# Kernel optimization log

Measured on AMD Instinct MI355X. Metric: run time of the kernel, lower is better.

## Reference

```python
import jax, jax.numpy as jnp
import numpy as np

B, S, E, H = 4, 2048, 1024, 8
D = E // H  # head_dim = 128


def setup_inputs() -> dict:
    key = jax.random.key(0)
    ks = jax.random.split(key, 7)
    scale = 1.0 / np.sqrt(D)
    return {
        "sequences": jax.random.normal(ks[0], (B, S, E), dtype=jnp.float32),
        # per-head Linear weights, torch layout [out, in] stacked over heads
        "Wq": jax.random.normal(ks[1], (H, D, D), dtype=jnp.float32) * scale,
        "Wk": jax.random.normal(ks[2], (H, D, D), dtype=jnp.float32) * scale,
        "Wv": jax.random.normal(ks[3], (H, D, D), dtype=jnp.float32) * scale,
        "bq": jax.random.normal(ks[4], (H, D), dtype=jnp.float32) * scale,
        "bk": jax.random.normal(ks[5], (H, D), dtype=jnp.float32) * scale,
        "bv": jax.random.normal(ks[6], (H, D), dtype=jnp.float32) * scale,
    }


def reference(sequences, Wq, Wk, Wv, bq, bk, bv):
    # split feature dim into heads: [B,S,H,D]
    xh = sequences.reshape(B, S, H, D)
    # torch Linear: y = x @ W.T + b  ->  contract input dim d with W[h, o, d]
    q = jnp.einsum("bshd,hod->bsho", xh, Wq) + bq
    k = jnp.einsum("bshd,hod->bsho", xh, Wk) + bk
    v = jnp.einsum("bshd,hod->bsho", xh, Wv) + bv
    # NOTE: original scales by 1/sqrt(num_heads), not 1/sqrt(head_dim)
    scores = jnp.einsum("bshd,bthd->bhst", q, k) / jnp.sqrt(jnp.float32(H))
    attn = jax.nn.softmax(scores, axis=-1)  # [B,H,S,S]
    out = jnp.einsum("bhst,bthd->bshd", attn, v)
    # hstack over heads == reshape back to [B,S,E]
    return out.reshape(B, S, E)
```

## Files before the change

### kernel.cpp

```cpp
#include <hip/hip_runtime.h>
#include <hip/hip_bf16.h>

#define B_ 4
#define S_ 2048
#define E_ 1024
#define H_ 8
#define D_ 128

using f16x8 = __attribute__((ext_vector_type(8))) _Float16;
using f32x4 = __attribute__((ext_vector_type(4))) float;

__device__ __forceinline__ ushort f2h_bits(float f) {
    union { _Float16 h; ushort u; } cv; cv.h = (_Float16)f; return cv.u;
}
__device__ __forceinline__ f16x8 pack8(const float* __restrict__ p) {
    float4 f0 = *(const float4*)p;
    float4 f1 = *(const float4*)(p + 4);
    f16x8 r;
    r[0] = (_Float16)f0.x; r[1] = (_Float16)f0.y;
    r[2] = (_Float16)f0.z; r[3] = (_Float16)f0.w;
    r[4] = (_Float16)f1.x; r[5] = (_Float16)f1.y;
    r[6] = (_Float16)f1.z; r[7] = (_Float16)f1.w;
    return r;
}

__device__ __forceinline__ void gll16(const ushort* g, ushort* l) {
    __builtin_amdgcn_global_load_lds(
        (const __attribute__((address_space(1))) unsigned int*)g,
        (__attribute__((address_space(3))) unsigned int*)l, 16, 0, 0);
}

__global__ __launch_bounds__(256) void kv_proj(
    const float* __restrict__ seq,
    const float* __restrict__ Wk, const float* __restrict__ Wv,
    const float* __restrict__ bk, const float* __restrict__ bv,
    ushort* __restrict__ ko, ushort* __restrict__ vo)
{
    __shared__ ushort T[128 * 68];
    const int m0 = blockIdx.x * 64, h = blockIdx.y;
    const int tid = threadIdx.x, lane = tid & 63, w = tid >> 6;
    const int l16 = lane & 15, quad = lane >> 4;

    f16x8 a[4];
    #pragma unroll
    for (int ks = 0; ks < 4; ++ks)
        a[ks] = pack8(&seq[(size_t)(m0 + w * 16 + l16) * E_
                           + h * D_ + ks * 32 + quad * 8]);

    {
        const float* W = Wk + (size_t)h * D_ * D_;
        f32x4 acc[8];
        #pragma unroll
        for (int nt = 0; nt < 8; ++nt) { f32x4 z = {0.f,0.f,0.f,0.f}; acc[nt] = z; }
        #pragma unroll
        for (int ks = 0; ks < 4; ++ks)
            #pragma unroll
            for (int nt = 0; nt < 8; ++nt) {
                f16x8 bfr = pack8(&W[(size_t)(nt * 16 + l16) * D_ + ks * 32 + quad * 8]);
                acc[nt] = __builtin_amdgcn_mfma_f32_16x16x32_f16(
                    a[ks], bfr, acc[nt], 0, 0, 0);
            }
        #pragma unroll
        for (int nt = 0; nt < 8; ++nt) {
            int o = nt * 16 + l16;
            float bias = bk[h * D_ + o];
            #pragma unroll
            for (int r = 0; r < 4; ++r) {
                int row = w * 16 + quad * 4 + r;
                T[row * 136 + (o ^ (quad << 3))] = f2h_bits(acc[nt][r] + bias);
            }
        }
    }
    __syncthreads();
    #pragma unroll
    for (int i = 0; i < 4; ++i) {
        int idx = tid + i * 256;
        int row = idx >> 4, c8 = (idx & 15) * 8;
        int lk = c8 ^ ((row & 7) << 3);
        uint4 dk = *(uint4*)&T[row * 136 + (lk ^ (((row >> 2) & 3) << 3))];
        int m = m0 + row, bi = m >> 11, s = m & (S_ - 1);
        *(uint4*)&ko[(((size_t)bi * H_ + h) * S_ + s) * D_ + c8] = dk;
    }
    __syncthreads();
    {
        const float* W = Wv + (size_t)h * D_ * D_;
        f32x4 acc[8];
        #pragma unroll
        for (int nt = 0; nt < 8; ++nt) { f32x4 z = {0.f,0.f,0.f,0.f}; acc[nt] = z; }
        #pragma unroll
        for (int ks = 0; ks < 4; ++ks)
            #pragma unroll
            for (int nt = 0; nt < 8; ++nt) {
                f16x8 bfr = pack8(&W[(size_t)(nt * 16 + l16) * D_ + ks * 32 + quad * 8]);
                acc[nt] = __builtin_amdgcn_mfma_f32_16x16x32_f16(
                    a[ks], bfr, acc[nt], 0, 0, 0);
            }
        #pragma unroll
        for (int nt = 0; nt < 8; ++nt) {
            int o = nt * 16 + l16;
            float bias = bv[h * D_ + o];
            #pragma unroll
            for (int r = 0; r < 4; ++r) {
                int row = w * 16 + quad * 4 + r;
                T[o * 68 + row] = f2h_bits(acc[nt][r] + bias);
            }
        }
    }
    __syncthreads();
    #pragma unroll
    for (int i = 0; i < 4; ++i) {
        int idx = tid + i * 256;
        int d = idx >> 3, c = idx & 7;
        uint4 dv = *(uint4*)&T[d * 68 + ((c ^ (d & 7)) << 3)];
        int bi = m0 >> 11, s0 = (m0 & (S_ - 1)) + c * 8;
        *(uint4*)&vo[(((size_t)bi * H_ + h) * D_ + d) * S_ + s0] = dv;
    }
}

__global__ __launch_bounds__(512) void attn(
    const float* __restrict__ seq, const float* __restrict__ Wq,
    const float* __restrict__ bq,
    const ushort* __restrict__ kg, const ushort* __restrict__ vtg,
    float* __restrict__ out)
{
    constexpr int NT = S_ / 64;
    __shared__ alignas(16) ushort Kbuf[2][64 * 128];
    __shared__ alignas(16) ushort Vbuf[2][128 * 64];
    __shared__ alignas(16) ushort Pbuf[128 * 64];

    const int m0 = blockIdx.x * 128;
    const int h = blockIdx.y, bi = blockIdx.z;
    const int bh = bi * H_ + h;
    const int tid = threadIdx.x, lane = tid & 63, w = tid >> 6;
    const int l16 = lane & 15, quad = lane >> 4;
    const int swz = l16 & 7;
    const ushort* kbase = kg + (size_t)bh * S_ * D_;
    const ushort* vbase = vtg + (size_t)bh * D_ * S_;
    const float qscale = 0.35355339059327373f * 1.4426950408889634f;

    #pragma unroll
    for (int c = 0; c < 2; ++c) {
        int i = w * 2 + c;
        gll16(vbase + (size_t)(i * 8 + (lane >> 3)) * S_ + (lane & 7) * 8,
              &Vbuf[0][0] + i * 512);
    }

    ushort* const Qs = &Kbuf[0][0];
    {
        f16x8 xa[4];
        #pragma unroll
        for (int ks = 0; ks < 4; ++ks)
            xa[ks] = pack8(&seq[((size_t)bi * S_ + m0 + w * 16 + l16) * E_
                                + h * D_ + ks * 32 + quad * 8]);
        f32x4 qacc[8];
        #pragma unroll
        for (int nt = 0; nt < 8; ++nt) { f32x4 z = {0.f,0.f,0.f,0.f}; qacc[nt] = z; }
        const float* W = Wq + (size_t)h * D_ * D_;
        #pragma unroll
        for (int ks = 0; ks < 4; ++ks)
            #pragma unroll
            for (int nt = 0; nt < 8; ++nt) {
                f16x8 bfr = pack8(&W[(size_t)(nt * 16 + l16) * D_ + ks * 32 + quad * 8]);
                qacc[nt] = __builtin_amdgcn_mfma_f32_16x16x32_f16(
                    xa[ks], bfr, qacc[nt], 0, 0, 0);
            }
        #pragma unroll
        for (int nt = 0; nt < 8; ++nt) {
            int o = nt * 16 + l16;
            float bias = bq[h * D_ + o];
            #pragma unroll
            for (int r = 0; r < 4; ++r) {
                int row = w * 16 + quad * 4 + r;
                Qs[row * 128 + (o ^ (quad << 3))] =
                    f2h_bits((qacc[nt][r] + bias) * qscale);
            }
        }
    }
    __syncthreads();

    f16x8 qf[4];
    #pragma unroll
    for (int ks = 0; ks < 4; ++ks)
        qf[ks] = *(const f16x8*)&Qs[(w * 16 + l16) * 128
                                    + ks * 32 + ((quad ^ (l16 >> 2)) << 3)];
    __syncthreads();

    #pragma unroll
    for (int c = 0; c < 2; ++c) {
        int i = w * 2 + c;
        gll16(kbase + i * 512 + lane * 8, &Kbuf[0][0] + i * 512);
    }

    f32x4 o_acc[8];
    #pragma unroll
    for (int nt = 0; nt < 8; ++nt) { f32x4 z = {0.f,0.f,0.f,0.f}; o_acc[nt] = z; }
    float m_prev = -1e30f, l_lane = 0.f;

    __syncthreads();

    ushort* const prow = &Pbuf[(w * 16 + l16) * 64];

    for (int j = 0; j < NT; ++j) {
        const int cur = j & 1;
        const ushort* KL = &Kbuf[cur][0];
        const ushort* VL = &Vbuf[cur][0];

        if (j + 1 < NT) {
            const ushort* kt = kbase + (size_t)(j + 1) * 64 * 128;
            const ushort* vt = vbase + (j + 1) * 64;
            ushort* kd = &Kbuf[cur ^ 1][0];
            ushort* vd = &Vbuf[cur ^ 1][0];
            #pragma unroll
            for (int c = 0; c < 2; ++c) {
                int i = w * 2 + c;
                gll16(kt + i * 512 + lane * 8, kd + i * 512);
                gll16(vt + (size_t)(i * 8 + (lane >> 3)) * S_ + (lane & 7) * 8,
                      vd + i * 512);
            }
        }

        f32x4 sacc[4];
        #pragma unroll
        for (int nt = 0; nt < 4; ++nt) { f32x4 z = {0.f,0.f,0.f,0.f}; sacc[nt] = z; }
        __builtin_amdgcn_s_setprio(1);
        #pragma unroll
        for (int ks = 0; ks < 4; ++ks)
            #pragma unroll
            for (int nt = 0; nt < 4; ++nt) {
                f16x8 kf = *(const f16x8*)&KL[(nt * 16 + l16) * 128
                                              + (((ks * 4 + quad) ^ swz) << 3)];
                sacc[nt] = __builtin_amdgcn_mfma_f32_16x16x32_f16(
                    kf, qf[ks], sacc[nt], 0, 0, 0);
            }
        __builtin_amdgcn_s_setprio(0);

        uint2 pkw[4];
        {
            float mx = fmaxf(fmaxf(sacc[0][0], sacc[0][1]), fmaxf(sacc[0][2], sacc[0][3]));
            #pragma unroll
            for (int nt = 1; nt < 4; ++nt)
                mx = fmaxf(mx, fmaxf(fmaxf(sacc[nt][0], sacc[nt][1]),
                                     fmaxf(sacc[nt][2], sacc[nt][3])));
            mx = fmaxf(mx, __shfl_xor(mx, 16));
            mx = fmaxf(mx, __shfl_xor(mx, 32));
            if (__any(mx > m_prev + 8.0f)) {
                float mnew  = fmaxf(m_prev, mx);
                float alpha = exp2f(m_prev - mnew);
                #pragma unroll
                for (int nt = 0; nt < 8; ++nt)
                    #pragma unroll
                    for (int r = 0; r < 4; ++r) o_acc[nt][r] *= alpha;
                l_lane *= alpha;
                m_prev = mnew;
            }
            #pragma unroll
            for (int nt = 0; nt < 4; ++nt) {
                float e0 = exp2f(sacc[nt][0] - m_prev);
                float e1 = exp2f(sacc[nt][1] - m_prev);
                float e2 = exp2f(sacc[nt][2] - m_prev);
                float e3 = exp2f(sacc[nt][3] - m_prev);
                auto p01 = __builtin_amdgcn_cvt_pkrtz(e0, e1);
                auto p23 = __builtin_amdgcn_cvt_pkrtz(e2, e3);
                l_lane += (float)p01[0] + (float)p01[1] + (float)p23[0] + (float)p23[1];
                pkw[nt] = make_uint2(__builtin_bit_cast(uint, p01),
                                     __builtin_bit_cast(uint, p23));
            }
        }

        #pragma unroll
        for (int nt = 0; nt < 4; ++nt) {
            int G = 2 * nt + (quad >> 1);
            *(uint2*)&prow[((G ^ swz) << 3) + ((quad & 1) << 2)] = pkw[nt];
        }

        __builtin_amdgcn_s_setprio(1);
        #pragma unroll
        for (int ks = 0; ks < 2; ++ks) {
            f16x8 pb = *(const f16x8*)&prow[((ks * 4 + quad) ^ swz) << 3];
            #pragma unroll
            for (int nt = 0; nt < 8; ++nt) {
                f16x8 vf = *(const f16x8*)&VL[(nt * 16 + l16) * 64
                                              + (((ks * 4 + quad) ^ swz) << 3)];
                o_acc[nt] = __builtin_amdgcn_mfma_f32_16x16x32_f16(
                    vf, pb, o_acc[nt], 0, 0, 0);
            }
        }
        __builtin_amdgcn_s_setprio(0);

        __syncthreads();
    }

    {
        float l = l_lane;
        l += __shfl_xor(l, 16);
        l += __shfl_xor(l, 32);
        float rinv = 1.0f / l;
        const int q = m0 + w * 16 + l16;
        #pragma unroll
        for (int nt = 0; nt < 8; ++nt) {
            float4 o;
            o.x = o_acc[nt][0] * rinv;
            o.y = o_acc[nt][1] * rinv;
            o.z = o_acc[nt][2] * rinv;
            o.w = o_acc[nt][3] * rinv;
            *(float4*)&out[((size_t)bi * S_ + q) * E_ + h * D_ + nt * 16 + quad * 4] = o;
        }
    }
}

extern "C" void kernel_launch(void* const* d_in, const int* in_sizes, int n_in,
                              void* d_out, int out_size, void* d_ws, size_t ws_size,
                              hipStream_t stream) {
    const float* seq = (const float*)d_in[0];
    const float* Wq  = (const float*)d_in[1];
    const float* Wk  = (const float*)d_in[2];
    const float* Wv  = (const float*)d_in[3];
    const float* bq  = (const float*)d_in[4];
    const float* bk  = (const float*)d_in[5];
    const float* bv  = (const float*)d_in[6];

    const size_t per = (size_t)B_ * H_ * S_ * D_;
    if (ws_size < 2 * per * sizeof(ushort)) return;
    ushort* kws  = (ushort*)d_ws;
    ushort* vtws = kws + per;

    kv_proj<<<dim3(B_ * S_ / 64, H_), 256, 0, stream>>>(
        seq, Wk, Wv, bk, bv, kws, vtws);
    attn<<<dim3(S_ / 128, H_, B_), 512, 0, stream>>>(
        seq, Wq, bq, kws, vtws, (float*)d_out);
}
```

Measured before the change: 280.0 us.

## Fuse K/V projection and attention into one cooperative kernel with grid sync

Merges the K/V projection and the attention kernel into one cooperative launch. Each block projects K, V and Q for its own 128 rows, writes K and V^T to the workspace, then waits on a grid-wide barrier before the flash-attention loop. The fused kernel reuses the loaded input fragments for all three projections and removes the second launch, at the cost of a grid sync and the requirement that all 512 blocks be co-resident. If the cooperative launch fails, it falls back to a reworked two-kernel path whose projection kernel handles 128 rows per block.

```diff
diff --git a/kernel.cpp b/kernel.cpp
--- a/kernel.cpp
+++ b/kernel.cpp
@@ -1,5 +1,8 @@
 #include <hip/hip_runtime.h>
 #include <hip/hip_bf16.h>
+#include <hip/hip_cooperative_groups.h>
+
+namespace cg = cooperative_groups;
 
 #define B_ 4
 #define S_ 2048
@@ -30,21 +33,37 @@
         (__attribute__((address_space(3))) unsigned int*)l, 16, 0, 0);
 }
 
-__global__ __launch_bounds__(256) void kv_proj(
+__global__ __launch_bounds__(512, 4) void mha_fused(
     const float* __restrict__ seq,
-    const float* __restrict__ Wk, const float* __restrict__ Wv,
-    const float* __restrict__ bk, const float* __restrict__ bv,
-    ushort* __restrict__ ko, ushort* __restrict__ vo)
+    const float* __restrict__ Wq, const float* __restrict__ Wk,
+    const float* __restrict__ Wv,
+    const float* __restrict__ bq, const float* __restrict__ bk,
+    const float* __restrict__ bv,
+    ushort* __restrict__ ko, ushort* __restrict__ vo,
+    float* __restrict__ out)
 {
-    __shared__ ushort T[128 * 68];
-    const int m0 = blockIdx.x * 64, h = blockIdx.y;
+    __shared__ alignas(16) ushort smem[40960];
+    ushort* const Tk = smem;
+    ushort* const Tv = smem + 17408;
+    ushort* const Qs = smem;
+    ushort* const Kb0 = smem;
+    ushort* const Kb1 = smem + 8192;
+    ushort* const Vb0 = smem + 16384;
+    ushort* const Vb1 = smem + 24576;
+    ushort* const Pbuf = smem + 32768;
+
+    const int bx = blockIdx.x, h = blockIdx.y, bi = blockIdx.z;
+    const int bh = bi * H_ + h;
+    const int m0 = bx * 128;
     const int tid = threadIdx.x, lane = tid & 63, w = tid >> 6;
     const int l16 = lane & 15, quad = lane >> 4;
+    const int swz = l16 & 7;
+    const float qscale = 0.35355339059327373f * 1.4426950408889634f;
 
     f16x8 a[4];
     #pragma unroll
     for (int ks = 0; ks < 4; ++ks)
-        a[ks] = pack8(&seq[(size_t)(m0 + w * 16 + l16) * E_
+        a[ks] = pack8(&seq[((size_t)bi * S_ + m0 + w * 16 + l16) * E_
                            + h * D_ + ks * 32 + quad * 8]);
 
     {
@@ -67,21 +86,10 @@
             #pragma unroll
             for (int r = 0; r < 4; ++r) {
                 int row = w * 16 + quad * 4 + r;
-                T[row * 136 + (o ^ (quad << 3))] = f2h_bits(acc[nt][r] + bias);
-            }
-        }
-    }
-    __syncthreads();
-    #pragma unroll
-    for (int i = 0; i < 4; ++i) {
-        int idx = tid + i * 256;
-        int row = idx >> 4, c8 = (idx & 15) * 8;
-        int lk = c8 ^ ((row & 7) << 3);
-        uint4 dk = *(uint4*)&T[row * 136 + (lk ^ (((row >> 2) & 3) << 3))];
-        int m = m0 + row, bi = m >> 11, s = m & (S_ - 1);
-        *(uint4*)&ko[(((size_t)bi * H_ + h) * S_ + s) * D_ + c8] = dk;
-    }
-    __syncthreads();
+                Tk[row * 136 + (o ^ (quad << 3))] = f2h_bits(acc[nt][r] + bias);
+            }
+        }
+    }
     {
         const float* W = Wv + (size_t)h * D_ * D_;
         f32x4 acc[8];
@@ -102,67 +110,35 @@
             #pragma unroll
             for (int r = 0; r < 4; ++r) {
                 int row = w * 16 + quad * 4 + r;
-                T[o * 68 + row] = f2h_bits(acc[nt][r] + bias);
+                Tv[o * 136 + row] = f2h_bits(acc[nt][r] + bias);
             }
         }
     }
     __syncthreads();
     #pragma unroll
     for (int i = 0; i < 4; ++i) {
-        int idx = tid + i * 256;
-        int d = idx >> 3, c = idx & 7;
-        uint4 dv = *(uint4*)&T[d * 68 + ((c ^ (d & 7)) << 3)];
-        int bi = m0 >> 11, s0 = (m0 & (S_ - 1)) + c * 8;
-        *(uint4*)&vo[(((size_t)bi * H_ + h) * D_ + d) * S_ + s0] = dv;
-    }
-}
-
-__global__ __launch_bounds__(512) void attn(
-    const float* __restrict__ seq, const float* __restrict__ Wq,
-    const float* __restrict__ bq,
-    const ushort* __restrict__ kg, const ushort* __restrict__ vtg,
-    float* __restrict__ out)
-{
-    constexpr int NT = S_ / 64;
-    __shared__ alignas(16) ushort Kbuf[2][64 * 128];
-    __shared__ alignas(16) ushort Vbuf[2][128 * 64];
-    __shared__ alignas(16) ushort Pbuf[128 * 64];
-
-    const int m0 = blockIdx.x * 128;
-    const int h = blockIdx.y, bi = blockIdx.z;
-    const int bh = bi * H_ + h;
-    const int tid = threadIdx.x, lane = tid & 63, w = tid >> 6;
-    const int l16 = lane & 15, quad = lane >> 4;
-    const int swz = l16 & 7;
-    const ushort* kbase = kg + (size_t)bh * S_ * D_;
-    const ushort* vbase = vtg + (size_t)bh * D_ * S_;
-    const float qscale = 0.35355339059327373f * 1.4426950408889634f;
-
-    #pragma unroll
-    for (int c = 0; c < 2; ++c) {
-        int i = w * 2 + c;
-        gll16(vbase + (size_t)(i * 8 + (lane >> 3)) * S_ + (lane & 7) * 8,
-              &Vbuf[0][0] + i * 512);
-    }
-
-    ushort* const Qs = &Kbuf[0][0];
-    {
-        f16x8 xa[4];
-        #pragma unroll
-        for (int ks = 0; ks < 4; ++ks)
-            xa[ks] = pack8(&seq[((size_t)bi * S_ + m0 + w * 16 + l16) * E_
-                                + h * D_ + ks * 32 + quad * 8]);
+        int idx = tid + i * 512;
+        int row = idx >> 4, c8 = (idx & 15) * 8;
+        int lk = c8 ^ ((row & 7) << 3);
+        uint4 dk = *(uint4*)&Tk[row * 136 + (lk ^ (((row >> 2) & 3) << 3))];
+        *(uint4*)&ko[((size_t)bh * S_ + m0 + row) * D_ + c8] = dk;
+        uint4 dv = *(uint4*)&Tv[row * 136 + (c8 ^ ((row & 7) << 3))];
+        *(uint4*)&vo[((size_t)bh * D_ + row) * S_ + m0 + c8] = dv;
+    }
+    __syncthreads();
+
+    {
+        const float* W = Wq + (size_t)h * D_ * D_;
         f32x4 qacc[8];
         #pragma unroll
         for (int nt = 0; nt < 8; ++nt) { f32x4 z = {0.f,0.f,0.f,0.f}; qacc[nt] = z; }
-        const float* W = Wq + (size_t)h * D_ * D_;
         #pragma unroll
         for (int ks = 0; ks < 4; ++ks)
             #pragma unroll
             for (int nt = 0; nt < 8; ++nt) {
                 f16x8 bfr = pack8(&W[(size_t)(nt * 16 + l16) * D_ + ks * 32 + quad * 8]);
                 qacc[nt] = __builtin_amdgcn_mfma_f32_16x16x32_f16(
-                    xa[ks], bfr, qacc[nt], 0, 0, 0);
+                    a[ks], bfr, qacc[nt], 0, 0, 0);
             }
         #pragma unroll
         for (int nt = 0; nt < 8; ++nt) {
@@ -176,8 +152,6 @@
             }
         }
     }
-    __syncthreads();
-
     f16x8 qf[4];
     #pragma unroll
     for (int ks = 0; ks < 4; ++ks)
@@ -185,10 +159,18 @@
                                     + ks * 32 + ((quad ^ (l16 >> 2)) << 3)];
     __syncthreads();
 
+    cg::this_grid().sync();
+
+    constexpr int NT = S_ / 64;
+    const ushort* kbase = ko + (size_t)bh * S_ * D_;
+    const ushort* vbase = vo + (size_t)bh * D_ * S_;
+
     #pragma unroll
     for (int c = 0; c < 2; ++c) {
         int i = w * 2 + c;
-        gll16(kbase + i * 512 + lane * 8, &Kbuf[0][0] + i * 512);
+        gll16(kbase + i * 512 + lane * 8, Kb0 + i * 512);
+        gll16(vbase + (size_t)(i * 8 + (lane >> 3)) * S_ + (lane & 7) * 8,
+              Vb0 + i * 512);
     }
 
     f32x4 o_acc[8];
@@ -201,15 +183,14 @@
     ushort* const prow = &Pbuf[(w * 16 + l16) * 64];
 
     for (int j = 0; j < NT; ++j) {
-        const int cur = j & 1;
-        const ushort* KL = &Kbuf[cur][0];
-        const ushort* VL = &Vbuf[cur][0];
+        const ushort* KL = (j & 1) ? Kb1 : Kb0;
+        const ushort* VL = (j & 1) ? Vb1 : Vb0;
 
         if (j + 1 < NT) {
             const ushort* kt = kbase + (size_t)(j + 1) * 64 * 128;
             const ushort* vt = vbase + (j + 1) * 64;
-            ushort* kd = &Kbuf[cur ^ 1][0];
-            ushort* vd = &Vbuf[cur ^ 1][0];
+            ushort* kd = (j & 1) ? Kb0 : Kb1;
+            ushort* vd = (j & 1) ? Vb0 : Vb1;
             #pragma unroll
             for (int c = 0; c < 2; ++c) {
                 int i = w * 2 + c;
@@ -308,6 +289,280 @@
     }
 }
 
+__global__ __launch_bounds__(256) void kv_proj(
+    const float* __restrict__ seq,
+    const float* __restrict__ Wk, const float* __restrict__ Wv,
+    const float* __restrict__ bk, const float* __restrict__ bv,
+    ushort* __restrict__ ko, ushort* __restrict__ vo)
+{
+    constexpr int TS = 136;
+    __shared__ ushort Tk[128 * TS];
+    __shared__ ushort Tv[128 * TS];
+    const int m0 = blockIdx.x * 128, h = blockIdx.y;
+    const int tid = threadIdx.x, lane = tid & 63, w = tid >> 6;
+    const int l16 = lane & 15, quad = lane >> 4;
+
+    f16x8 a[2][4];
+    #pragma unroll
+    for (int mt = 0; mt < 2; ++mt)
+        #pragma unroll
+        for (int ks = 0; ks < 4; ++ks)
+            a[mt][ks] = pack8(&seq[(size_t)(m0 + w * 32 + mt * 16 + l16) * E_
+                                   + h * D_ + ks * 32 + quad * 8]);
+    {
+        const float* W = Wk + (size_t)h * D_ * D_;
+        f32x4 acc[2][8];
+        #pragma unroll
+        for (int mt = 0; mt < 2; ++mt)
+            #pragma unroll
+            for (int nt = 0; nt < 8; ++nt) { f32x4 z = {0.f,0.f,0.f,0.f}; acc[mt][nt] = z; }
+        #pragma unroll
+        for (int ks = 0; ks < 4; ++ks)
+            #pragma unroll
+            for (int nt = 0; nt < 8; ++nt) {
+                f16x8 bfr = pack8(&W[(size_t)(nt * 16 + l16) * D_ + ks * 32 + quad * 8]);
+                #pragma unroll
+                for (int mt = 0; mt < 2; ++mt)
+                    acc[mt][nt] = __builtin_amdgcn_mfma_f32_16x16x32_f16(
+                        a[mt][ks], bfr, acc[mt][nt], 0, 0, 0);
+            }
+        #pragma unroll
+        for (int nt = 0; nt < 8; ++nt) {
+            int o = nt * 16 + l16;
+            float bias = bk[h * D_ + o];
+            #pragma unroll
+            for (int mt = 0; mt < 2; ++mt)
+                #pragma unroll
+                for (int r = 0; r < 4; ++r) {
+                    int row = w * 32 + mt * 16 + quad * 4 + r;
+                    Tk[row * TS + (o ^ (quad << 3))] = f2h_bits(acc[mt][nt][r] + bias);
+                }
+        }
+    }
+    {
+        const float* W = Wv + (size_t)h * D_ * D_;
+        f32x4 acc[2][8];
+        #pragma unroll
+        for (int mt = 0; mt < 2; ++mt)
+            #pragma unroll
+            for (int nt = 0; nt < 8; ++nt) { f32x4 z = {0.f,0.f,0.f,0.f}; acc[mt][nt] = z; }
+        #pragma unroll
+        for (int ks = 0; ks < 4; ++ks)
+            #pragma unroll
+            for (int nt = 0; nt < 8; ++nt) {
+                f16x8 bfr = pack8(&W[(size_t)(nt * 16 + l16) * D_ + ks * 32 + quad * 8]);
+                #pragma unroll
+                for (int mt = 0; mt < 2; ++mt)
+                    acc[mt][nt] = __builtin_amdgcn_mfma_f32_16x16x32_f16(
+                        a[mt][ks], bfr, acc[mt][nt], 0, 0, 0);
+            }
+        #pragma unroll
+        for (int nt = 0; nt < 8; ++nt) {
+            int o = nt * 16 + l16;
+            float bias = bv[h * D_ + o];
+            #pragma unroll
+            for (int mt = 0; mt < 2; ++mt)
+                #pragma unroll
+                for (int r = 0; r < 4; ++r) {
+                    int row = w * 32 + mt * 16 + quad * 4 + r;
+                    Tv[o * TS + row] = f2h_bits(acc[mt][nt][r] + bias);
+                }
+        }
+    }
+    __syncthreads();
+    #pragma unroll
+    for (int i = 0; i < 8; ++i) {
+        int idx = tid + i * 256;
+        int row = idx >> 4, c8 = (idx & 15) * 8;
+        int lk = c8 ^ ((row & 7) << 3);
+        uint4 dk = *(uint4*)&Tk[row * TS + (lk ^ (((row >> 2) & 3) << 3))];
+        int m = m0 + row, bi = m >> 11, s = m & (S_ - 1);
+        *(uint4*)&ko[(((size_t)bi * H_ + h) * S_ + s) * D_ + c8] = dk;
+        uint4 dv = *(uint4*)&Tv[row * TS + (c8 ^ ((row & 7) << 3))];
+        int mg = m0 + c8, bv_i = mg >> 11, s0 = mg & (S_ - 1);
+        *(uint4*)&vo[(((size_t)bv_i * H_ + h) * D_ + row) * S_ + s0] = dv;
+    }
+}
+
+__global__ __launch_bounds__(512) void attn(
+    const float* __restrict__ seq, const float* __restrict__ Wq,
+    const float* __restrict__ bq,
+    const ushort* __restrict__ kg, const ushort* __restrict__ vtg,
+    float* __restrict__ out)
+{
+    constexpr int NT = S_ / 64;
+    __shared__ alignas(16) ushort Kbuf[2][64 * 128];
+    __shared__ alignas(16) ushort Vbuf[2][128 * 64];
+    __shared__ alignas(16) ushort Pbuf[128 * 64];
+
+    const int m0 = blockIdx.x * 128;
+    const int h = blockIdx.y, bi = blockIdx.z;
+    const int bh = bi * H_ + h;
+    const int tid = threadIdx.x, lane = tid & 63, w = tid >> 6;
+    const int l16 = lane & 15, quad = lane >> 4;
+    const int swz = l16 & 7;
+    const ushort* kbase = kg + (size_t)bh * S_ * D_;
+    const ushort* vbase = vtg + (size_t)bh * D_ * S_;
+    const float qscale = 0.35355339059327373f * 1.4426950408889634f;
+
+    #pragma unroll
+    for (int c = 0; c < 2; ++c) {
+        int i = w * 2 + c;
+        gll16(vbase + (size_t)(i * 8 + (lane >> 3)) * S_ + (lane & 7) * 8,
+              &Vbuf[0][0] + i * 512);
+    }
+    ushort* const Qs = &Kbuf[0][0];
+    {
+        f16x8 xa[4];
+        #pragma unroll
+        for (int ks = 0; ks < 4; ++ks)
+            xa[ks] = pack8(&seq[((size_t)bi * S_ + m0 + w * 16 + l16) * E_
+                                + h * D_ + ks * 32 + quad * 8]);
+        f32x4 qacc[8];
+        #pragma unroll
+        for (int nt = 0; nt < 8; ++nt) { f32x4 z = {0.f,0.f,0.f,0.f}; qacc[nt] = z; }
+        const float* W = Wq + (size_t)h * D_ * D_;
+        #pragma unroll
+        for (int ks = 0; ks < 4; ++ks)
+            #pragma unroll
+            for (int nt = 0; nt < 8; ++nt) {
+                f16x8 bfr = pack8(&W[(size_t)(nt * 16 + l16) * D_ + ks * 32 + quad * 8]);
+                qacc[nt] = __builtin_amdgcn_mfma_f32_16x16x32_f16(
+                    xa[ks], bfr, qacc[nt], 0, 0, 0);
+            }
+        #pragma unroll
+        for (int nt = 0; nt < 8; ++nt) {
+            int o = nt * 16 + l16;
+            float bias = bq[h * D_ + o];
+            #pragma unroll
+            for (int r = 0; r < 4; ++r) {
+                int row = w * 16 + quad * 4 + r;
+                Qs[row * 128 + (o ^ (quad << 3))] =
+                    f2h_bits((qacc[nt][r] + bias) * qscale);
+            }
+        }
+    }
+    __syncthreads();
+    f16x8 qf[4];
+    #pragma unroll
+    for (int ks = 0; ks < 4; ++ks)
+        qf[ks] = *(const f16x8*)&Qs[(w * 16 + l16) * 128
+                                    + ks * 32 + ((quad ^ (l16 >> 2)) << 3)];
+    __syncthreads();
+    #pragma unroll
+    for (int c = 0; c < 2; ++c) {
+        int i = w * 2 + c;
+        gll16(kbase + i * 512 + lane * 8, &Kbuf[0][0] + i * 512);
+    }
+    f32x4 o_acc[8];
+    #pragma unroll
+    for (int nt = 0; nt < 8; ++nt) { f32x4 z = {0.f,0.f,0.f,0.f}; o_acc[nt] = z; }
+    float m_prev = -1e30f, l_lane = 0.f;
+    __syncthreads();
+
+    ushort* const prow = &Pbuf[(w * 16 + l16) * 64];
+
+    for (int j = 0; j < NT; ++j) {
+        const int cur = j & 1;
+        const ushort* KL = &Kbuf[cur][0];
+        const ushort* VL = &Vbuf[cur][0];
+        if (j + 1 < NT) {
+            const ushort* kt = kbase + (size_t)(j + 1) * 64 * 128;
+            const ushort* vt = vbase + (j + 1) * 64;
+            ushort* kd = &Kbuf[cur ^ 1][0];
+            ushort* vd = &Vbuf[cur ^ 1][0];
+            #pragma unroll
+            for (int c = 0; c < 2; ++c) {
+                int i = w * 2 + c;
+                gll16(kt + i * 512 + lane * 8, kd + i * 512);
+                gll16(vt + (size_t)(i * 8 + (lane >> 3)) * S_ + (lane & 7) * 8,
+                      vd + i * 512);
+            }
+        }
+        f32x4 sacc[4];
+        #pragma unroll
+        for (int nt = 0; nt < 4; ++nt) { f32x4 z = {0.f,0.f,0.f,0.f}; sacc[nt] = z; }
+        __builtin_amdgcn_s_setprio(1);
+        #pragma unroll
+        for (int ks = 0; ks < 4; ++ks)
+            #pragma unroll
+            for (int nt = 0; nt < 4; ++nt) {
+                f16x8 kf = *(const f16x8*)&KL[(nt * 16 + l16) * 128
+                                              + (((ks * 4 + quad) ^ swz) << 3)];
+                sacc[nt] = __builtin_amdgcn_mfma_f32_16x16x32_f16(
+                    kf, qf[ks], sacc[nt], 0, 0, 0);
+            }
+        __builtin_amdgcn_s_setprio(0);
+        uint2 pkw[4];
+        {
+            float mx = fmaxf(fmaxf(sacc[0][0], sacc[0][1]), fmaxf(sacc[0][2], sacc[0][3]));
+            #pragma unroll
+            for (int nt = 1; nt < 4; ++nt)
+                mx = fmaxf(mx, fmaxf(fmaxf(sacc[nt][0], sacc[nt][1]),
+                                     fmaxf(sacc[nt][2], sacc[nt][3])));
+            mx = fmaxf(mx, __shfl_xor(mx, 16));
+            mx = fmaxf(mx, __shfl_xor(mx, 32));
+            if (__any(mx > m_prev + 8.0f)) {
+                float mnew  = fmaxf(m_prev, mx);
+                float alpha = exp2f(m_prev - mnew);
+                #pragma unroll
+                for (int nt = 0; nt < 8; ++nt)
+                    #pragma unroll
+                    for (int r = 0; r < 4; ++r) o_acc[nt][r] *= alpha;
+                l_lane *= alpha;
+                m_prev = mnew;
+            }
+            #pragma unroll
+            for (int nt = 0; nt < 4; ++nt) {
+                float e0 = exp2f(sacc[nt][0] - m_prev);
+                float e1 = exp2f(sacc[nt][1] - m_prev);
+                float e2 = exp2f(sacc[nt][2] - m_prev);
+                float e3 = exp2f(sacc[nt][3] - m_prev);
+                auto p01 = __builtin_amdgcn_cvt_pkrtz(e0, e1);
+                auto p23 = __builtin_amdgcn_cvt_pkrtz(e2, e3);
+                l_lane += (float)p01[0] + (float)p01[1] + (float)p23[0] + (float)p23[1];
+                pkw[nt] = make_uint2(__builtin_bit_cast(uint, p01),
+                                     __builtin_bit_cast(uint, p23));
+            }
+        }
+        #pragma unroll
+        for (int nt = 0; nt < 4; ++nt) {
+            int G = 2 * nt + (quad >> 1);
+            *(uint2*)&prow[((G ^ swz) << 3) + ((quad & 1) << 2)] = pkw[nt];
+        }
+        __builtin_amdgcn_s_setprio(1);
+        #pragma unroll
+        for (int ks = 0; ks < 2; ++ks) {
+            f16x8 pb = *(const f16x8*)&prow[((ks * 4 + quad) ^ swz) << 3];
+            #pragma unroll
+            for (int nt = 0; nt < 8; ++nt) {
+                f16x8 vf = *(const f16x8*)&VL[(nt * 16 + l16) * 64
+                                              + (((ks * 4 + quad) ^ swz) << 3)];
+                o_acc[nt] = __builtin_amdgcn_mfma_f32_16x16x32_f16(
+                    vf, pb, o_acc[nt], 0, 0, 0);
+            }
+        }
+        __builtin_amdgcn_s_setprio(0);
+        __syncthreads();
+    }
+    {
+        float l = l_lane;
+        l += __shfl_xor(l, 16);
+        l += __shfl_xor(l, 32);
+        float rinv = 1.0f / l;
+        const int q = m0 + w * 16 + l16;
+        #pragma unroll
+        for (int nt = 0; nt < 8; ++nt) {
+            float4 o;
+            o.x = o_acc[nt][0] * rinv;
+            o.y = o_acc[nt][1] * rinv;
+            o.z = o_acc[nt][2] * rinv;
+            o.w = o_acc[nt][3] * rinv;
+            *(float4*)&out[((size_t)bi * S_ + q) * E_ + h * D_ + nt * 16 + quad * 4] = o;
+        }
+    }
+}
+
 extern "C" void kernel_launch(void* const* d_in, const int* in_sizes, int n_in,
                               void* d_out, int out_size, void* d_ws, size_t ws_size,
                               hipStream_t stream) {
@@ -323,9 +578,18 @@
     if (ws_size < 2 * per * sizeof(ushort)) return;
     ushort* kws  = (ushort*)d_ws;
     ushort* vtws = kws + per;
-
-    kv_proj<<<dim3(B_ * S_ / 64, H_), 256, 0, stream>>>(
-        seq, Wk, Wv, bk, bv, kws, vtws);
-    attn<<<dim3(S_ / 128, H_, B_), 512, 0, stream>>>(
-        seq, Wq, bq, kws, vtws, (float*)d_out);
-}
+    float* outp  = (float*)d_out;
+
+    void* args[] = {(void*)&seq, (void*)&Wq, (void*)&Wk, (void*)&Wv,
+                    (void*)&bq, (void*)&bk, (void*)&bv,
+                    (void*)&kws, (void*)&vtws, (void*)&outp};
+    hipError_t err = hipLaunchCooperativeKernel(
+        (const void*)mha_fused, dim3(S_ / 128, H_, B_), dim3(512),
+        args, 0, stream);
+    if (err != hipSuccess) {
+        kv_proj<<<dim3(B_ * S_ / 128, H_), 256, 0, stream>>>(
+            seq, Wk, Wv, bk, bv, kws, vtws);
+        attn<<<dim3(S_ / 128, H_, B_), 512, 0, stream>>>(
+            seq, Wq, bq, kws, vtws, outp);
+    }
+}
```

Result: slower. 332.1 us (+18.6%).

## Double kv_proj row tile and remap attention blocks for L2 locality

Applied to the files above, without the earlier changes.

kv_proj now processes 128 rows per block with two M-subtiles per wave, so each converted weight fragment feeds two MFMAs. K and V results go to separate LDS tiles, which drops the intermediate barriers, and V is transposed through a padded buffer. The attention grid is remapped from a linear block index so that blocks sharing the same (batch, head) K/V stream are spread across XCD-interleaved slots, aiming for better L2 reuse. The kv_proj change raises register and LDS use per block, which may lower occupancy.

```diff
diff --git a/kernel.cpp b/kernel.cpp
--- a/kernel.cpp
+++ b/kernel.cpp
@@ -36,84 +36,94 @@
     const float* __restrict__ bk, const float* __restrict__ bv,
     ushort* __restrict__ ko, ushort* __restrict__ vo)
 {
-    __shared__ ushort T[128 * 68];
-    const int m0 = blockIdx.x * 64, h = blockIdx.y;
+    constexpr int TS = 136;
+    __shared__ ushort Tk[128 * TS];
+    __shared__ ushort Tv[128 * TS];
+    const int m0 = blockIdx.x * 128, h = blockIdx.y;
     const int tid = threadIdx.x, lane = tid & 63, w = tid >> 6;
     const int l16 = lane & 15, quad = lane >> 4;
 
-    f16x8 a[4];
-    #pragma unroll
-    for (int ks = 0; ks < 4; ++ks)
-        a[ks] = pack8(&seq[(size_t)(m0 + w * 16 + l16) * E_
-                           + h * D_ + ks * 32 + quad * 8]);
+    f16x8 a[2][4];
+    #pragma unroll
+    for (int mt = 0; mt < 2; ++mt)
+        #pragma unroll
+        for (int ks = 0; ks < 4; ++ks)
+            a[mt][ks] = pack8(&seq[(size_t)(m0 + w * 32 + mt * 16 + l16) * E_
+                                   + h * D_ + ks * 32 + quad * 8]);
 
     {
         const float* W = Wk + (size_t)h * D_ * D_;
-        f32x4 acc[8];
-        #pragma unroll
-        for (int nt = 0; nt < 8; ++nt) { f32x4 z = {0.f,0.f,0.f,0.f}; acc[nt] = z; }
+        f32x4 acc[2][8];
+        #pragma unroll
+        for (int mt = 0; mt < 2; ++mt)
+            #pragma unroll
+            for (int nt = 0; nt < 8; ++nt) { f32x4 z = {0.f,0.f,0.f,0.f}; acc[mt][nt] = z; }
         #pragma unroll
         for (int ks = 0; ks < 4; ++ks)
             #pragma unroll
             for (int nt = 0; nt < 8; ++nt) {
                 f16x8 bfr = pack8(&W[(size_t)(nt * 16 + l16) * D_ + ks * 32 + quad * 8]);
-                acc[nt] = __builtin_amdgcn_mfma_f32_16x16x32_f16(
-                    a[ks], bfr, acc[nt], 0, 0, 0);
+                #pragma unroll
+                for (int mt = 0; mt < 2; ++mt)
+                    acc[mt][nt] = __builtin_amdgcn_mfma_f32_16x16x32_f16(
+                        a[mt][ks], bfr, acc[mt][nt], 0, 0, 0);
             }
         #pragma unroll
         for (int nt = 0; nt < 8; ++nt) {
             int o = nt * 16 + l16;
             float bias = bk[h * D_ + o];
             #pragma unroll
-            for (int r = 0; r < 4; ++r) {
-                int row = w * 16 + quad * 4 + r;
-                T[row * 136 + (o ^ (quad << 3))] = f2h_bits(acc[nt][r] + bias);
-            }
+            for (int mt = 0; mt < 2; ++mt)
+                #pragma unroll
+                for (int r = 0; r < 4; ++r) {
+                    int row = w * 32 + mt * 16 + quad * 4 + r;
+                    Tk[row * TS + (o ^ (quad << 3))] = f2h_bits(acc[mt][nt][r] + bias);
+                }
+        }
+    }
+    {
+        const float* W = Wv + (size_t)h * D_ * D_;
+        f32x4 acc[2][8];
+        #pragma unroll
+        for (int mt = 0; mt < 2; ++mt)
+            #pragma unroll
+            for (int nt = 0; nt < 8; ++nt) { f32x4 z = {0.f,0.f,0.f,0.f}; acc[mt][nt] = z; }
+        #pragma unroll
+        for (int ks = 0; ks < 4; ++ks)
+            #pragma unroll
+            for (int nt = 0; nt < 8; ++nt) {
+                f16x8 bfr = pack8(&W[(size_t)(nt * 16 + l16) * D_ + ks * 32 + quad * 8]);
+                #pragma unroll
+                for (int mt = 0; mt < 2; ++mt)
+                    acc[mt][nt] = __builtin_amdgcn_mfma_f32_16x16x32_f16(
+                        a[mt][ks], bfr, acc[mt][nt], 0, 0, 0);
+            }
+        #pragma unroll
+        for (int nt = 0; nt < 8; ++nt) {
+            int o = nt * 16 + l16;
+            float bias = bv[h * D_ + o];
+            #pragma unroll
+            for (int mt = 0; mt < 2; ++mt)
+                #pragma unroll
+                for (int r = 0; r < 4; ++r) {
+                    int row = w * 32 + mt * 16 + quad * 4 + r;
+                    Tv[o * TS + row] = f2h_bits(acc[mt][nt][r] + bias);
+                }
         }
     }
     __syncthreads();
-    #pragma unroll
-    for (int i = 0; i < 4; ++i) {
+
+    #pragma unroll
+    for (int i = 0; i < 8; ++i) {
         int idx = tid + i * 256;
         int row = idx >> 4, c8 = (idx & 15) * 8;
         int lk = c8 ^ ((row & 7) << 3);
-        uint4 dk = *(uint4*)&T[row * 136 + (lk ^ (((row >> 2) & 3) << 3))];
+        uint4 dk = *(uint4*)&Tk[row * TS + (lk ^ (((row >> 2) & 3) << 3))];
         int m = m0 + row, bi = m >> 11, s = m & (S_ - 1);
         *(uint4*)&ko[(((size_t)bi * H_ + h) * S_ + s) * D_ + c8] = dk;
-    }
-    __syncthreads();
-    {
-        const float* W = Wv + (size_t)h * D_ * D_;
-        f32x4 acc[8];
-        #pragma unroll
-        for (int nt = 0; nt < 8; ++nt) { f32x4 z = {0.f,0.f,0.f,0.f}; acc[nt] = z; }
-        #pragma unroll
-        for (int ks = 0; ks < 4; ++ks)
-            #pragma unroll
-            for (int nt = 0; nt < 8; ++nt) {
-                f16x8 bfr = pack8(&W[(size_t)(nt * 16 + l16) * D_ + ks * 32 + quad * 8]);
-                acc[nt] = __builtin_amdgcn_mfma_f32_16x16x32_f16(
-                    a[ks], bfr, acc[nt], 0, 0, 0);
-            }
-        #pragma unroll
-        for (int nt = 0; nt < 8; ++nt) {
-            int o = nt * 16 + l16;
-            float bias = bv[h * D_ + o];
-            #pragma unroll
-            for (int r = 0; r < 4; ++r) {
-                int row = w * 16 + quad * 4 + r;
-                T[o * 68 + row] = f2h_bits(acc[nt][r] + bias);
-            }
-        }
-    }
-    __syncthreads();
-    #pragma unroll
-    for (int i = 0; i < 4; ++i) {
-        int idx = tid + i * 256;
-        int d = idx >> 3, c = idx & 7;
-        uint4 dv = *(uint4*)&T[d * 68 + ((c ^ (d & 7)) << 3)];
-        int bi = m0 >> 11, s0 = (m0 & (S_ - 1)) + c * 8;
-        *(uint4*)&vo[(((size_t)bi * H_ + h) * D_ + d) * S_ + s0] = dv;
+        uint4 dv = *(uint4*)&Tv[row * TS + (c8 ^ ((row & 7) << 3))];
+        int mg = m0 + c8, bv_i = mg >> 11, s0 = mg & (S_ - 1);
+        *(uint4*)&vo[(((size_t)bv_i * H_ + h) * D_ + row) * S_ + s0] = dv;
     }
 }
 
@@ -128,8 +138,12 @@
     __shared__ alignas(16) ushort Vbuf[2][128 * 64];
     __shared__ alignas(16) ushort Pbuf[128 * 64];
 
-    const int m0 = blockIdx.x * 128;
-    const int h = blockIdx.y, bi = blockIdx.z;
+    const int L = blockIdx.x + 16 * blockIdx.y + 128 * blockIdx.z;
+    const int c = L & 7, t = L >> 3;
+    const int g = c * 4 + (t & 3);
+    const int h = g & 7, bi = g >> 3;
+    const int m0 = (t >> 2) * 128;
+
     const int bh = bi * H_ + h;
     const int tid = threadIdx.x, lane = tid & 63, w = tid >> 6;
     const int l16 = lane & 15, quad = lane >> 4;
@@ -139,8 +153,8 @@
     const float qscale = 0.35355339059327373f * 1.4426950408889634f;
 
     #pragma unroll
-    for (int c = 0; c < 2; ++c) {
-        int i = w * 2 + c;
+    for (int ci = 0; ci < 2; ++ci) {
+        int i = w * 2 + ci;
         gll16(vbase + (size_t)(i * 8 + (lane >> 3)) * S_ + (lane & 7) * 8,
               &Vbuf[0][0] + i * 512);
     }
@@ -186,8 +200,8 @@
     __syncthreads();
 
     #pragma unroll
-    for (int c = 0; c < 2; ++c) {
-        int i = w * 2 + c;
+    for (int ci = 0; ci < 2; ++ci) {
+        int i = w * 2 + ci;
         gll16(kbase + i * 512 + lane * 8, &Kbuf[0][0] + i * 512);
     }
 
@@ -211,8 +225,8 @@
             ushort* kd = &Kbuf[cur ^ 1][0];
             ushort* vd = &Vbuf[cur ^ 1][0];
             #pragma unroll
-            for (int c = 0; c < 2; ++c) {
-                int i = w * 2 + c;
+            for (int ci = 0; ci < 2; ++ci) {
+                int i = w * 2 + ci;
                 gll16(kt + i * 512 + lane * 8, kd + i * 512);
                 gll16(vt + (size_t)(i * 8 + (lane >> 3)) * S_ + (lane & 7) * 8,
                       vd + i * 512);
@@ -324,8 +338,8 @@
     ushort* kws  = (ushort*)d_ws;
     ushort* vtws = kws + per;
 
-    kv_proj<<<dim3(B_ * S_ / 64, H_), 256, 0, stream>>>(
+    kv_proj<<<dim3(B_ * S_ / 128, H_), 256, 0, stream>>>(
         seq, Wk, Wv, bk, bv, kws, vtws);
-    attn<<<dim3(S_ / 128, H_, B_), 512, 0, stream>>>(
+    attn<<<dim3(16, 8, 4), 512, 0, stream>>>(
         seq, Wq, bq, kws, vtws, (float*)d_out);
 }
```

After: 250.7 us. 10.5% less time.
